# Performance work log

Hardware: AMD Instinct MI355X
Metric: run time of the kernel (lower is better)

Reference implementation:

```python
import jax, jax.numpy as jnp
import numpy as np

B, N, D = 2, 2048, 1024
H = 16
HD = D // H  # head_dim for kq and v

def setup_inputs() -> dict:
    key = jax.random.key(0)
    ks = jax.random.split(key, 5)
    scale = 1.0 / np.sqrt(D)
    return {
        "x": jax.random.normal(ks[0], (B, N, D), dtype=jnp.float32),
        "Wq": jax.random.normal(ks[1], (D, D), dtype=jnp.float32) * scale,
        "Wk": jax.random.normal(ks[2], (D, D), dtype=jnp.float32) * scale,
        "Wv": jax.random.normal(ks[3], (D, D), dtype=jnp.float32) * scale,
        "Wo": jax.random.normal(ks[4], (D, D), dtype=jnp.float32) * scale,
        "bo": jnp.zeros((D,), dtype=jnp.float32),
    }

def reference(x, Wq, Wk, Wv, Wo, bo):
    b, n, _ = x.shape
    # projections; torch Linear computes x @ W.T
    q = (x @ Wq.T).reshape(b, n, H, HD).transpose(0, 2, 1, 3)  # [B,H,N,HD]
    k = (x @ Wk.T).reshape(b, n, H, HD).transpose(0, 2, 1, 3)
    v = (x @ Wv.T).reshape(b, n, H, HD).transpose(0, 2, 1, 3)
    scores = jnp.einsum('bhqd,bhkd->bhqk', q, k) / jnp.sqrt(jnp.asarray(HD, x.dtype))
    causal = jnp.tril(jnp.ones((n, n), dtype=bool))
    scores = jnp.where(causal, scores, jnp.asarray(-jnp.inf, scores.dtype))
    probs = jax.nn.softmax(scores, axis=-1)  # dropout p=0.0 (eval)
    out = jnp.einsum('bhqk,bhkd->bhqd', probs, v)  # [B,H,N,HD]
    out = out.transpose(0, 2, 1, 3).reshape(b, n, D)
    return out @ Wo.T + bo
```

## Files before the change

kernel.cpp:

```cpp
#include <hip/hip_runtime.h>
#include <hip/hip_bf16.h>


typedef __bf16 bf16;
typedef __bf16 bf16x2 __attribute__((ext_vector_type(2)));
typedef __bf16 bf16x4 __attribute__((ext_vector_type(4)));
typedef __bf16 bf16x8 __attribute__((ext_vector_type(8)));
typedef float f32x4 __attribute__((ext_vector_type(4)));
typedef unsigned int u32x4 __attribute__((ext_vector_type(4)));

__device__ __forceinline__ f32x4 mfma16(bf16x8 a, bf16x8 b, f32x4 c) {
    return __builtin_amdgcn_mfma_f32_16x16x32_bf16(a, b, c, 0, 0, 0);
}

__device__ __forceinline__ void gload16(const bf16* g, bf16* l) {
    __builtin_amdgcn_global_load_lds(
        (const __attribute__((address_space(1))) unsigned int*)g,
        (__attribute__((address_space(3))) unsigned int*)l, 16, 0, 0);
}

__device__ __forceinline__ unsigned pk2(float a, float b) {
    bf16x2 v;
    v[0] = (bf16)a;
    v[1] = (bf16)b;
    return __builtin_bit_cast(unsigned, v);
}

__global__ __launch_bounds__(256) void f2b_kernel(const float* __restrict__ in,
                                                  bf16* __restrict__ out, int n) {
    int i = (blockIdx.x * 256 + threadIdx.x) * 4;
    if (i >= n) return;
    float4 v = *(const float4*)&in[i];
    bf16x4 o;
    o.x = (bf16)v.x; o.y = (bf16)v.y; o.z = (bf16)v.z; o.w = (bf16)v.w;
    *(bf16x4*)&out[i] = o;
}

__global__ __launch_bounds__(256) void w2b_kernel(
    const float* __restrict__ w0, const float* __restrict__ w1,
    const float* __restrict__ w2, const float* __restrict__ w3,
    bf16* __restrict__ o0, bf16* __restrict__ o1,
    bf16* __restrict__ o2, bf16* __restrict__ o3) {
    int sel = blockIdx.x >> 10;
    const float* in = sel == 0 ? w0 : sel == 1 ? w1 : sel == 2 ? w2 : w3;
    bf16* out = sel == 0 ? o0 : sel == 1 ? o1 : sel == 2 ? o2 : o3;
    int i = ((blockIdx.x & 1023) * 256 + threadIdx.x) * 4;
    float4 v = *(const float4*)&in[i];
    bf16x4 o;
    o.x = (bf16)v.x; o.y = (bf16)v.y; o.z = (bf16)v.z; o.w = (bf16)v.w;
    *(bf16x4*)&out[i] = o;
}

template <int MODE>
__device__ __forceinline__ void gemm_body(const bf16* __restrict__ A,
                                          const bf16* __restrict__ B,
                                          bf16* __restrict__ Cb,
                                          float* __restrict__ Cf,
                                          const float* __restrict__ bias,
                                          float scale, int N, int K, int row0, int col0) {
    __shared__ alignas(16) bf16 sA[128 * 32];
    __shared__ alignas(16) bf16 sB[128 * 32];
    const int tid  = threadIdx.x;
    const int lane = tid & 63;
    const int wave = tid >> 6;
    const int wrow = (wave >> 1) * 64;
    const int wcol = (wave & 1) * 64;
    const int la = lane & 15, lb = lane >> 4;

    const f32x4 fzero = {0.f, 0.f, 0.f, 0.f};
    f32x4 acc[4][4];
#pragma unroll
    for (int m = 0; m < 4; ++m)
#pragma unroll
        for (int n = 0; n < 4; ++n) acc[m][n] = fzero;

    for (int k0 = 0; k0 < K; k0 += 32) {
#pragma unroll
        for (int i = 0; i < 2; ++i) {
            int idx = i * 256 + tid;
            int r = idx >> 2, s = idx & 3;
            gload16(&A[(size_t)(row0 + r) * K + k0 + s * 8], &sA[idx * 8]);
            gload16(&B[(size_t)(col0 + r) * K + k0 + s * 8], &sB[idx * 8]);
        }
        __syncthreads();
        bf16x8 af[4], bfv[4];
#pragma unroll
        for (int m = 0; m < 4; ++m)
            af[m] = *(const bf16x8*)&sA[(wrow + m * 16 + la) * 32 + lb * 8];
#pragma unroll
        for (int n = 0; n < 4; ++n)
            bfv[n] = *(const bf16x8*)&sB[(wcol + n * 16 + la) * 32 + lb * 8];
#pragma unroll
        for (int m = 0; m < 4; ++m)
#pragma unroll
            for (int n = 0; n < 4; ++n)
                acc[m][n] = mfma16(af[m], bfv[n], acc[m][n]);
        __syncthreads();
    }
#pragma unroll
    for (int m = 0; m < 4; ++m)
#pragma unroll
        for (int n = 0; n < 4; ++n) {
            int col = col0 + wcol + n * 16 + la;
            if (MODE == 2) {
                int hh = col >> 6, hd = col & 63;
                int hc = hd >> 4, lav = hd & 15;
                int sp = row0 + wrow + m * 16 + lb * 4;
                int ktile = sp >> 6, k = sp & 63;
                int c = k >> 4, q = k & 15;
                size_t addr = (size_t)(ktile * 16 + hh) * 4096 +
                              (size_t)(((hc * 2 + (c >> 1)) * 16 + lav) * 32 +
                                       (q >> 2) * 8 + (c & 1) * 4);
                bf16x4 o4;
#pragma unroll
                for (int r = 0; r < 4; ++r) o4[r] = (bf16)acc[m][n][r];
                *(bf16x4*)&Cb[addr] = o4;
            } else if (MODE == 3) {
                int hh = col >> 6, hd = col & 63;
#pragma unroll
                for (int r = 0; r < 4; ++r) {
                    int row = row0 + wrow + m * 16 + lb * 4 + r;
                    int ktile = row >> 6, key = row & 63;
                    size_t addr = (size_t)(ktile * 16 + hh) * 4096 +
                                  (size_t)((((key >> 4) * 2 + (hd >> 5)) * 16 +
                                            (key & 15)) * 32 +
                                           ((hd >> 3) & 3) * 8 + (hd & 7));
                    Cb[addr] = (bf16)acc[m][n][r];
                }
            } else {
#pragma unroll
                for (int r = 0; r < 4; ++r) {
                    int row = row0 + wrow + m * 16 + lb * 4 + r;
                    if (MODE == 1)
                        Cf[(size_t)row * N + col] = acc[m][n][r] + bias[col];
                    else
                        Cb[(size_t)row * N + col] = (bf16)(acc[m][n][r] * scale);
                }
            }
        }
}

__global__ __launch_bounds__(256) void gemm_qkv_kernel(
    const bf16* __restrict__ xb, const bf16* __restrict__ wq,
    const bf16* __restrict__ wk, const bf16* __restrict__ wv,
    bf16* __restrict__ Q, bf16* __restrict__ Kf, bf16* __restrict__ Vf) {
    int z = blockIdx.z;
    if (z == 2) {
        gemm_body<2>(xb, wv, Vf, nullptr, nullptr, 1.f, 1024, 1024,
                     blockIdx.x * 128, blockIdx.y * 128);
    } else if (z == 1) {
        gemm_body<3>(xb, wk, Kf, nullptr, nullptr, 1.f, 1024, 1024,
                     blockIdx.x * 128, blockIdx.y * 128);
    } else {
        gemm_body<0>(xb, wq, Q, nullptr, nullptr, 0.1803368801111204f, 1024, 1024,
                     blockIdx.x * 128, blockIdx.y * 128);
    }
}

__global__ __launch_bounds__(256) void gemm_out_kernel(
    const bf16* __restrict__ att, const bf16* __restrict__ wo,
    float* __restrict__ out, const float* __restrict__ bias) {
    gemm_body<1>(att, wo, nullptr, out, bias, 1.f, 1024, 1024,
                 blockIdx.x * 128, blockIdx.y * 128);
}

struct KF { bf16x8 f[4][2]; };

__global__ __launch_bounds__(256, 2) void attn_kernel(
    const bf16* __restrict__ Q, const bf16* __restrict__ Kf,
    const bf16* __restrict__ Vf, bf16* __restrict__ O) {
    const int lane = threadIdx.x & 63;
    const int wave = threadIdx.x >> 6;
    const int bid = blockIdx.x;
    const int bh = (bid & 7) * 4 + ((bid >> 3) & 3);
    const int slot = bid >> 5;
    const int qt = slot < 8 ? slot : 23 - slot;
    const int h = bh & 15;
    const int b = bh >> 4;
    const int q0w = qt * 128 + wave * 32;
    const int rowbase = b * 2048;
    const int la = lane & 15, lb = lane >> 4;
    const f32x4 fzero = {0.f, 0.f, 0.f, 0.f};
    const float C = 14.426950408889634f;
    const int colbase = h * 64;
    const int lane_off = la * 32 + lb * 8;
    const int TSTRIDE = 16 * 4096;

    bf16x8 aq[2][2];
#pragma unroll
    for (int mf = 0; mf < 2; ++mf) {
        const bf16* qp = &Q[(size_t)(rowbase + q0w + mf * 16 + la) * 1024 + colbase];
#pragma unroll
        for (int kc = 0; kc < 2; ++kc) aq[mf][kc] = *(const bf16x8*)(qp + kc * 32 + lb * 8);
    }

    bf16x8 bones;
#pragma unroll
    for (int j = 0; j < 8; ++j) bones[j] = (bf16)1.0f;

    f32x4 o[2][4], lacc[2];
#pragma unroll
    for (int mf = 0; mf < 2; ++mf) {
        lacc[mf] = fzero;
#pragma unroll
        for (int hc = 0; hc < 4; ++hc) o[mf][hc] = fzero;
    }

    const int nt = (q0w + 95) >> 6;

    const bf16* kbase = &Kf[(size_t)(b * 32 * 16 + h) * 4096 + lane_off + 2048];
    const bf16* vbase = &Vf[(size_t)(b * 32 * 16 + h) * 4096 + lane_off + 2048];

    KF ka, kb, va, vb;
#pragma unroll
    for (int ck = 0; ck < 4; ++ck) {
        ka.f[ck][0] = *(const bf16x8*)(kbase + (ck * 2 + 0) * 512 - 2048);
        ka.f[ck][1] = *(const bf16x8*)(kbase + (ck * 2 + 1) * 512 - 2048);
        va.f[ck][0] = *(const bf16x8*)(vbase + (ck * 2 + 0) * 512 - 2048);
        va.f[ck][1] = *(const bf16x8*)(vbase + (ck * 2 + 1) * 512 - 2048);
    }
    const bf16* kpf = kbase + (nt > 1 ? TSTRIDE : 0);
    const bf16* vpf = vbase + (nt > 1 ? TSTRIDE : 0);

    auto TILE = [&](int t, KF& kc, KF& kn, KF& vc, KF& vn) {
        const bool domask = (t == nt - 1);
#pragma unroll
        for (int ck = 0; ck < 4; ++ck) {
            kn.f[ck][0] = *(const bf16x8*)(kpf + (ck * 2 + 0) * 512 - 2048);
            kn.f[ck][1] = *(const bf16x8*)(kpf + (ck * 2 + 1) * 512 - 2048);
            vn.f[ck][0] = *(const bf16x8*)(vpf + (ck * 2 + 0) * 512 - 2048);
            vn.f[ck][1] = *(const bf16x8*)(vpf + (ck * 2 + 1) * 512 - 2048);
        }
        int adv = (t + 2 < nt) ? TSTRIDE : 0;
        kpf += adv;
        vpf += adv;
        f32x4 s[2][4];
#pragma unroll
        for (int mf = 0; mf < 2; ++mf)
#pragma unroll
            for (int ck = 0; ck < 4; ++ck) s[mf][ck] = fzero;
        __builtin_amdgcn_s_setprio(1);
#pragma unroll
        for (int ck = 0; ck < 4; ++ck)
#pragma unroll
            for (int mf = 0; mf < 2; ++mf) {
                s[mf][ck] = mfma16(kc.f[ck][0], aq[mf][0], s[mf][ck]);
                s[mf][ck] = mfma16(kc.f[ck][1], aq[mf][1], s[mf][ck]);
            }
        __builtin_amdgcn_s_setprio(0);
        if (domask) {
            const int k0 = t * 64;
#pragma unroll
            for (int mf = 0; mf < 2; ++mf) {
                int qrow = q0w + mf * 16 + la;
#pragma unroll
                for (int ck = 0; ck < 4; ++ck)
#pragma unroll
                    for (int r = 0; r < 4; ++r) {
                        int key = k0 + ck * 16 + lb * 4 + r;
                        if (key > qrow) s[mf][ck][r] = -1e30f;
                    }
            }
        }
        bf16x8 pa[2][2];
#pragma unroll
        for (int mf = 0; mf < 2; ++mf) {
            unsigned pk[4][2];
#pragma unroll
            for (int ck = 0; ck < 4; ++ck) {
                float p0 = __builtin_amdgcn_exp2f(s[mf][ck][0] - C);
                float p1 = __builtin_amdgcn_exp2f(s[mf][ck][1] - C);
                float p2 = __builtin_amdgcn_exp2f(s[mf][ck][2] - C);
                float p3 = __builtin_amdgcn_exp2f(s[mf][ck][3] - C);
                pk[ck][0] = pk2(p0, p1);
                pk[ck][1] = pk2(p2, p3);
            }
#pragma unroll
            for (int kc2 = 0; kc2 < 2; ++kc2) {
                u32x4 w;
                w.x = pk[kc2 * 2][0];
                w.y = pk[kc2 * 2][1];
                w.z = pk[kc2 * 2 + 1][0];
                w.w = pk[kc2 * 2 + 1][1];
                pa[mf][kc2] = __builtin_bit_cast(bf16x8, w);
            }
        }
        __builtin_amdgcn_s_setprio(1);
#pragma unroll
        for (int hc = 0; hc < 4; ++hc)
#pragma unroll
            for (int mf = 0; mf < 2; ++mf) {
                o[mf][hc] = mfma16(pa[mf][0], vc.f[hc][0], o[mf][hc]);
                o[mf][hc] = mfma16(pa[mf][1], vc.f[hc][1], o[mf][hc]);
            }
#pragma unroll
        for (int mf = 0; mf < 2; ++mf) {
            lacc[mf] = mfma16(pa[mf][0], bones, lacc[mf]);
            lacc[mf] = mfma16(pa[mf][1], bones, lacc[mf]);
        }
        __builtin_amdgcn_s_setprio(0);
    };

    int t = 0;
    for (; t + 2 <= nt; t += 2) {
        TILE(t, ka, kb, va, vb);
        TILE(t + 1, kb, ka, vb, va);
    }
    if (t < nt) TILE(t, ka, kb, va, vb);

#pragma unroll
    for (int mf = 0; mf < 2; ++mf)
#pragma unroll
        for (int hc = 0; hc < 4; ++hc)
#pragma unroll
            for (int r = 0; r < 4; ++r) {
                int qrow = q0w + mf * 16 + lb * 4 + r;
                O[(size_t)(rowbase + qrow) * 1024 + colbase + hc * 16 + la] =
                    (bf16)(o[mf][hc][r] / lacc[mf][r]);
            }
}

extern "C" void kernel_launch(void* const* d_in, const int* in_sizes, int n_in,
                              void* d_out, int out_size, void* d_ws, size_t ws_size,
                              hipStream_t stream) {
    const float* x  = (const float*)d_in[0];
    const float* Wq = (const float*)d_in[1];
    const float* Wk = (const float*)d_in[2];
    const float* Wv = (const float*)d_in[3];
    const float* Wo = (const float*)d_in[4];
    const float* bo = (const float*)d_in[5];
    float* out = (float*)d_out;

    char* ws = (char*)d_ws;
    const size_t MB = 1024 * 1024;
    bf16* xb  = (bf16*)(ws + (size_t)0);
    bf16* wqb = (bf16*)(ws + 8 * MB);
    bf16* wkb = (bf16*)(ws + 10 * MB);
    bf16* wvb = (bf16*)(ws + 12 * MB);
    bf16* wob = (bf16*)(ws + 14 * MB);
    bf16* Qb  = (bf16*)(ws + 16 * MB);
    bf16* Kf  = (bf16*)(ws + 24 * MB);
    bf16* Vf  = (bf16*)(ws + 40 * MB);
    bf16* Ab  = (bf16*)(ws + 56 * MB);

    f2b_kernel<<<4096, 256, 0, stream>>>(x, xb, 4096 * 1024);
    w2b_kernel<<<4096, 256, 0, stream>>>(Wq, Wk, Wv, Wo, wqb, wkb, wvb, wob);

    gemm_qkv_kernel<<<dim3(32, 8, 3), 256, 0, stream>>>(xb, wqb, wkb, wvb, Qb, Kf, Vf);
    attn_kernel<<<512, 256, 0, stream>>>(Qb, Kf, Vf, Ab);
    gemm_out_kernel<<<dim3(32, 8), 256, 0, stream>>>(Ab, wob, out, bo);
}
```

Before: 102.6 us.

## Stage K/V tiles through LDS with double-buffered async global loads

The attention kernel stops having each wave load its own K and V fragments from global memory into registers. Instead the block cooperatively copies each 64-key K/V tile into double-buffered shared memory using global_load_lds, and every wave reads its fragments from LDS. To match, the pre-permuted K/V layouts written by the QKV GEMM are changed so that each 1 KB fragment is contiguous per lane. The intent is to cut redundant global traffic, since four waves share the same K/V, and to lower register pressure. In exchange it adds a block-wide barrier on every tile and runs the loop to the block's maximum tile count, so waves with fewer tiles sit idle.

```diff
diff --git a/kernel.cpp b/kernel.cpp
--- a/kernel.cpp
+++ b/kernel.cpp
@@ -107,10 +107,10 @@
                 int hc = hd >> 4, lav = hd & 15;
                 int sp = row0 + wrow + m * 16 + lb * 4;
                 int ktile = sp >> 6, k = sp & 63;
-                int c = k >> 4, q = k & 15;
+                int c = k >> 4, g = (k >> 2) & 3;
                 size_t addr = (size_t)(ktile * 16 + hh) * 4096 +
-                              (size_t)(((hc * 2 + (c >> 1)) * 16 + lav) * 32 +
-                                       (q >> 2) * 8 + (c & 1) * 4);
+                              (size_t)((hc * 2 + (c >> 1)) * 512 +
+                                       (lav + g * 16) * 8 + (c & 1) * 4);
                 bf16x4 o4;
 #pragma unroll
                 for (int r = 0; r < 4; ++r) o4[r] = (bf16)acc[m][n][r];
@@ -122,9 +122,9 @@
                     int row = row0 + wrow + m * 16 + lb * 4 + r;
                     int ktile = row >> 6, key = row & 63;
                     size_t addr = (size_t)(ktile * 16 + hh) * 4096 +
-                                  (size_t)((((key >> 4) * 2 + (hd >> 5)) * 16 +
-                                            (key & 15)) * 32 +
-                                           ((hd >> 3) & 3) * 8 + (hd & 7));
+                                  (size_t)(((key >> 4) * 2 + (hd >> 5)) * 512 +
+                                           ((key & 15) + ((hd >> 3) & 3) * 16) * 8 +
+                                           (hd & 7));
                     Cb[addr] = (bf16)acc[m][n][r];
                 }
             } else {
@@ -164,11 +164,10 @@
                  blockIdx.x * 128, blockIdx.y * 128);
 }
 
-struct KF { bf16x8 f[4][2]; };
-
 __global__ __launch_bounds__(256, 2) void attn_kernel(
     const bf16* __restrict__ Q, const bf16* __restrict__ Kf,
     const bf16* __restrict__ Vf, bf16* __restrict__ O) {
+    __shared__ alignas(16) char smem[32768];
     const int lane = threadIdx.x & 63;
     const int wave = threadIdx.x >> 6;
     const int bid = blockIdx.x;
@@ -183,8 +182,10 @@
     const f32x4 fzero = {0.f, 0.f, 0.f, 0.f};
     const float C = 14.426950408889634f;
     const int colbase = h * 64;
-    const int lane_off = la * 32 + lb * 8;
-    const int TSTRIDE = 16 * 4096;
+    const size_t TSTRIDE = 16 * 4096;
+
+    const bf16* kg = Kf + ((size_t)(b * 32) * 16 + h) * 4096 + lane * 8;
+    const bf16* vg = Vf + ((size_t)(b * 32) * 16 + h) * 4096 + lane * 8;
 
     bf16x8 aq[2][2];
 #pragma unroll
@@ -207,106 +208,104 @@
     }
 
     const int nt = (q0w + 95) >> 6;
-
-    const bf16* kbase = &Kf[(size_t)(b * 32 * 16 + h) * 4096 + lane_off + 2048];
-    const bf16* vbase = &Vf[(size_t)(b * 32 * 16 + h) * 4096 + lane_off + 2048];
-
-    KF ka, kb, va, vb;
-#pragma unroll
-    for (int ck = 0; ck < 4; ++ck) {
-        ka.f[ck][0] = *(const bf16x8*)(kbase + (ck * 2 + 0) * 512 - 2048);
-        ka.f[ck][1] = *(const bf16x8*)(kbase + (ck * 2 + 1) * 512 - 2048);
-        va.f[ck][0] = *(const bf16x8*)(vbase + (ck * 2 + 0) * 512 - 2048);
-        va.f[ck][1] = *(const bf16x8*)(vbase + (ck * 2 + 1) * 512 - 2048);
-    }
-    const bf16* kpf = kbase + (nt > 1 ? TSTRIDE : 0);
-    const bf16* vpf = vbase + (nt > 1 ? TSTRIDE : 0);
-
-    auto TILE = [&](int t, KF& kc, KF& kn, KF& vc, KF& vn) {
-        const bool domask = (t == nt - 1);
-#pragma unroll
-        for (int ck = 0; ck < 4; ++ck) {
-            kn.f[ck][0] = *(const bf16x8*)(kpf + (ck * 2 + 0) * 512 - 2048);
-            kn.f[ck][1] = *(const bf16x8*)(kpf + (ck * 2 + 1) * 512 - 2048);
-            vn.f[ck][0] = *(const bf16x8*)(vpf + (ck * 2 + 0) * 512 - 2048);
-            vn.f[ck][1] = *(const bf16x8*)(vpf + (ck * 2 + 1) * 512 - 2048);
+    const int ntmax = 2 * qt + 2;
+
+    auto STAGE = [&](int tile, int cur) {
+        const bf16* ks = kg + (size_t)tile * TSTRIDE;
+        const bf16* vs = vg + (size_t)tile * TSTRIDE;
+        char* dst = smem + cur * 16384;
+#pragma unroll
+        for (int i = 0; i < 2; ++i) {
+            int f = wave + i * 4;
+            gload16(ks + f * 512, (bf16*)(dst + f * 1024));
+            gload16(vs + f * 512, (bf16*)(dst + 8192 + f * 1024));
         }
-        int adv = (t + 2 < nt) ? TSTRIDE : 0;
-        kpf += adv;
-        vpf += adv;
-        f32x4 s[2][4];
-#pragma unroll
-        for (int mf = 0; mf < 2; ++mf)
-#pragma unroll
-            for (int ck = 0; ck < 4; ++ck) s[mf][ck] = fzero;
-        __builtin_amdgcn_s_setprio(1);
-#pragma unroll
-        for (int ck = 0; ck < 4; ++ck)
+    };
+
+    STAGE(0, 0);
+    __syncthreads();
+
+    int cur = 0;
+    for (int t = 0; t < ntmax; ++t) {
+        if (t + 1 < ntmax) STAGE(t + 1, cur ^ 1);
+        if (t < nt) {
+            const char* kbuf = smem + cur * 16384;
+            const char* vbuf = kbuf + 8192;
+            f32x4 s[2][4];
+#pragma unroll
+            for (int mf = 0; mf < 2; ++mf)
+#pragma unroll
+                for (int ck = 0; ck < 4; ++ck) s[mf][ck] = fzero;
+            __builtin_amdgcn_s_setprio(1);
+#pragma unroll
+            for (int ck = 0; ck < 4; ++ck) {
+                bf16x8 k0 = *(const bf16x8*)(kbuf + (ck * 2 + 0) * 1024 + lane * 16);
+                bf16x8 k1 = *(const bf16x8*)(kbuf + (ck * 2 + 1) * 1024 + lane * 16);
+#pragma unroll
+                for (int mf = 0; mf < 2; ++mf) {
+                    s[mf][ck] = mfma16(k0, aq[mf][0], s[mf][ck]);
+                    s[mf][ck] = mfma16(k1, aq[mf][1], s[mf][ck]);
+                }
+            }
+            __builtin_amdgcn_s_setprio(0);
+            if (t == nt - 1) {
+                const int k0r = t * 64;
+#pragma unroll
+                for (int mf = 0; mf < 2; ++mf) {
+                    int qrow = q0w + mf * 16 + la;
+#pragma unroll
+                    for (int ck = 0; ck < 4; ++ck)
+#pragma unroll
+                        for (int r = 0; r < 4; ++r) {
+                            int key = k0r + ck * 16 + lb * 4 + r;
+                            if (key > qrow) s[mf][ck][r] = -1e30f;
+                        }
+                }
+            }
+            bf16x8 pa[2][2];
 #pragma unroll
             for (int mf = 0; mf < 2; ++mf) {
-                s[mf][ck] = mfma16(kc.f[ck][0], aq[mf][0], s[mf][ck]);
-                s[mf][ck] = mfma16(kc.f[ck][1], aq[mf][1], s[mf][ck]);
-            }
-        __builtin_amdgcn_s_setprio(0);
-        if (domask) {
-            const int k0 = t * 64;
+                unsigned pk[4][2];
+#pragma unroll
+                for (int ck = 0; ck < 4; ++ck) {
+                    float p0 = __builtin_amdgcn_exp2f(s[mf][ck][0] - C);
+                    float p1 = __builtin_amdgcn_exp2f(s[mf][ck][1] - C);
+                    float p2 = __builtin_amdgcn_exp2f(s[mf][ck][2] - C);
+                    float p3 = __builtin_amdgcn_exp2f(s[mf][ck][3] - C);
+                    pk[ck][0] = pk2(p0, p1);
+                    pk[ck][1] = pk2(p2, p3);
+                }
+#pragma unroll
+                for (int kc2 = 0; kc2 < 2; ++kc2) {
+                    u32x4 w;
+                    w.x = pk[kc2 * 2][0];
+                    w.y = pk[kc2 * 2][1];
+                    w.z = pk[kc2 * 2 + 1][0];
+                    w.w = pk[kc2 * 2 + 1][1];
+                    pa[mf][kc2] = __builtin_bit_cast(bf16x8, w);
+                }
+            }
+            __builtin_amdgcn_s_setprio(1);
+#pragma unroll
+            for (int hc = 0; hc < 4; ++hc) {
+                bf16x8 v0 = *(const bf16x8*)(vbuf + (hc * 2 + 0) * 1024 + lane * 16);
+                bf16x8 v1 = *(const bf16x8*)(vbuf + (hc * 2 + 1) * 1024 + lane * 16);
+#pragma unroll
+                for (int mf = 0; mf < 2; ++mf) {
+                    o[mf][hc] = mfma16(pa[mf][0], v0, o[mf][hc]);
+                    o[mf][hc] = mfma16(pa[mf][1], v1, o[mf][hc]);
+                }
+            }
 #pragma unroll
             for (int mf = 0; mf < 2; ++mf) {
-                int qrow = q0w + mf * 16 + la;
-#pragma unroll
-                for (int ck = 0; ck < 4; ++ck)
-#pragma unroll
-                    for (int r = 0; r < 4; ++r) {
-                        int key = k0 + ck * 16 + lb * 4 + r;
-                        if (key > qrow) s[mf][ck][r] = -1e30f;
-                    }
-            }
+                lacc[mf] = mfma16(pa[mf][0], bones, lacc[mf]);
+                lacc[mf] = mfma16(pa[mf][1], bones, lacc[mf]);
+            }
+            __builtin_amdgcn_s_setprio(0);
         }
-        bf16x8 pa[2][2];
-#pragma unroll
-        for (int mf = 0; mf < 2; ++mf) {
-            unsigned pk[4][2];
-#pragma unroll
-            for (int ck = 0; ck < 4; ++ck) {
-                float p0 = __builtin_amdgcn_exp2f(s[mf][ck][0] - C);
-                float p1 = __builtin_amdgcn_exp2f(s[mf][ck][1] - C);
-                float p2 = __builtin_amdgcn_exp2f(s[mf][ck][2] - C);
-                float p3 = __builtin_amdgcn_exp2f(s[mf][ck][3] - C);
-                pk[ck][0] = pk2(p0, p1);
-                pk[ck][1] = pk2(p2, p3);
-            }
-#pragma unroll
-            for (int kc2 = 0; kc2 < 2; ++kc2) {
-                u32x4 w;
-                w.x = pk[kc2 * 2][0];
-                w.y = pk[kc2 * 2][1];
-                w.z = pk[kc2 * 2 + 1][0];
-                w.w = pk[kc2 * 2 + 1][1];
-                pa[mf][kc2] = __builtin_bit_cast(bf16x8, w);
-            }
-        }
-        __builtin_amdgcn_s_setprio(1);
-#pragma unroll
-        for (int hc = 0; hc < 4; ++hc)
-#pragma unroll
-            for (int mf = 0; mf < 2; ++mf) {
-                o[mf][hc] = mfma16(pa[mf][0], vc.f[hc][0], o[mf][hc]);
-                o[mf][hc] = mfma16(pa[mf][1], vc.f[hc][1], o[mf][hc]);
-            }
-#pragma unroll
-        for (int mf = 0; mf < 2; ++mf) {
-            lacc[mf] = mfma16(pa[mf][0], bones, lacc[mf]);
-            lacc[mf] = mfma16(pa[mf][1], bones, lacc[mf]);
-        }
-        __builtin_amdgcn_s_setprio(0);
-    };
-
-    int t = 0;
-    for (; t + 2 <= nt; t += 2) {
-        TILE(t, ka, kb, va, vb);
-        TILE(t + 1, kb, ka, vb, va);
-    }
-    if (t < nt) TILE(t, ka, kb, va, vb);
+        __syncthreads();
+        cur ^= 1;
+    }
 
 #pragma unroll
     for (int mf = 0; mf < 2; ++mf)
```

Measured after the change: 106.3 us. +3.6%, slower.

## Double-buffer GEMM LDS tiles and merge input conversion kernels into one launch

Applied to the files above, without the earlier changes.

The GEMM main loop now keeps two LDS buffers for the A and B tiles, so the asynchronous global-to-LDS load of the next K-slice is issued before the MFMA work on the current slice. This aims to hide global memory latency behind compute and uses one barrier per slice instead of two. Separately, the x and weight fp32-to-bf16 conversion kernels are fused into a single launch to save one kernel launch. The cost is double the LDS per block, which may reduce occupancy, and the loop assumes K is a multiple of 64.

```diff
diff --git a/kernel.cpp b/kernel.cpp
--- a/kernel.cpp
+++ b/kernel.cpp
@@ -26,25 +26,25 @@
     return __builtin_bit_cast(unsigned, v);
 }
 
-__global__ __launch_bounds__(256) void f2b_kernel(const float* __restrict__ in,
-                                                  bf16* __restrict__ out, int n) {
-    int i = (blockIdx.x * 256 + threadIdx.x) * 4;
-    if (i >= n) return;
-    float4 v = *(const float4*)&in[i];
-    bf16x4 o;
-    o.x = (bf16)v.x; o.y = (bf16)v.y; o.z = (bf16)v.z; o.w = (bf16)v.w;
-    *(bf16x4*)&out[i] = o;
-}
-
-__global__ __launch_bounds__(256) void w2b_kernel(
-    const float* __restrict__ w0, const float* __restrict__ w1,
-    const float* __restrict__ w2, const float* __restrict__ w3,
+__global__ __launch_bounds__(256) void conv_kernel(
+    const float* __restrict__ x, const float* __restrict__ w0,
+    const float* __restrict__ w1, const float* __restrict__ w2,
+    const float* __restrict__ w3, bf16* __restrict__ xb,
     bf16* __restrict__ o0, bf16* __restrict__ o1,
     bf16* __restrict__ o2, bf16* __restrict__ o3) {
-    int sel = blockIdx.x >> 10;
-    const float* in = sel == 0 ? w0 : sel == 1 ? w1 : sel == 2 ? w2 : w3;
-    bf16* out = sel == 0 ? o0 : sel == 1 ? o1 : sel == 2 ? o2 : o3;
-    int i = ((blockIdx.x & 1023) * 256 + threadIdx.x) * 4;
+    int blk = blockIdx.x;
+    const float* in;
+    bf16* out;
+    int base;
+    if (blk < 4096) {
+        in = x; out = xb; base = blk;
+    } else {
+        int sel = (blk - 4096) >> 10;
+        in = sel == 0 ? w0 : sel == 1 ? w1 : sel == 2 ? w2 : w3;
+        out = sel == 0 ? o0 : sel == 1 ? o1 : sel == 2 ? o2 : o3;
+        base = (blk - 4096) & 1023;
+    }
+    int i = (base * 256 + threadIdx.x) * 4;
     float4 v = *(const float4*)&in[i];
     bf16x4 o;
     o.x = (bf16)v.x; o.y = (bf16)v.y; o.z = (bf16)v.z; o.w = (bf16)v.w;
@@ -58,8 +58,8 @@
                                           float* __restrict__ Cf,
                                           const float* __restrict__ bias,
                                           float scale, int N, int K, int row0, int col0) {
-    __shared__ alignas(16) bf16 sA[128 * 32];
-    __shared__ alignas(16) bf16 sB[128 * 32];
+    __shared__ alignas(16) bf16 sA[2][128 * 32];
+    __shared__ alignas(16) bf16 sB[2][128 * 32];
     const int tid  = threadIdx.x;
     const int lane = tid & 63;
     const int wave = tid >> 6;
@@ -74,27 +74,38 @@
 #pragma unroll
         for (int n = 0; n < 4; ++n) acc[m][n] = fzero;
 
-    for (int k0 = 0; k0 < K; k0 += 32) {
+    auto STAGE = [&](int k0, int buf) {
 #pragma unroll
         for (int i = 0; i < 2; ++i) {
             int idx = i * 256 + tid;
             int r = idx >> 2, s = idx & 3;
-            gload16(&A[(size_t)(row0 + r) * K + k0 + s * 8], &sA[idx * 8]);
-            gload16(&B[(size_t)(col0 + r) * K + k0 + s * 8], &sB[idx * 8]);
-        }
-        __syncthreads();
+            gload16(&A[(size_t)(row0 + r) * K + k0 + s * 8], &sA[buf][idx * 8]);
+            gload16(&B[(size_t)(col0 + r) * K + k0 + s * 8], &sB[buf][idx * 8]);
+        }
+    };
+    auto COMPUTE = [&](int buf) {
         bf16x8 af[4], bfv[4];
 #pragma unroll
         for (int m = 0; m < 4; ++m)
-            af[m] = *(const bf16x8*)&sA[(wrow + m * 16 + la) * 32 + lb * 8];
+            af[m] = *(const bf16x8*)&sA[buf][(wrow + m * 16 + la) * 32 + lb * 8];
 #pragma unroll
         for (int n = 0; n < 4; ++n)
-            bfv[n] = *(const bf16x8*)&sB[(wcol + n * 16 + la) * 32 + lb * 8];
+            bfv[n] = *(const bf16x8*)&sB[buf][(wcol + n * 16 + la) * 32 + lb * 8];
 #pragma unroll
         for (int m = 0; m < 4; ++m)
 #pragma unroll
             for (int n = 0; n < 4; ++n)
                 acc[m][n] = mfma16(af[m], bfv[n], acc[m][n]);
+    };
+
+    STAGE(0, 0);
+    __syncthreads();
+    for (int k0 = 0; k0 < K; k0 += 64) {
+        if (k0 + 32 < K) STAGE(k0 + 32, 1);
+        COMPUTE(0);
+        __syncthreads();
+        if (k0 + 64 < K) STAGE(k0 + 64, 0);
+        COMPUTE(1);
         __syncthreads();
     }
 #pragma unroll
@@ -343,8 +354,7 @@
     bf16* Vf  = (bf16*)(ws + 40 * MB);
     bf16* Ab  = (bf16*)(ws + 56 * MB);
 
-    f2b_kernel<<<4096, 256, 0, stream>>>(x, xb, 4096 * 1024);
-    w2b_kernel<<<4096, 256, 0, stream>>>(Wq, Wk, Wv, Wo, wqb, wkb, wvb, wob);
+    conv_kernel<<<8192, 256, 0, stream>>>(x, Wq, Wk, Wv, Wo, xb, wqb, wkb, wvb, wob);
 
     gemm_qkv_kernel<<<dim3(32, 8, 3), 256, 0, stream>>>(xb, wqb, wkb, wvb, Qb, Kf, Vf);
     attn_kernel<<<512, 256, 0, stream>>>(Qb, Kf, Vf, Ab);
```

Result: slower. 131.1 us (+27.8%).
